# Optimization experiments

Measured on AMD Instinct MI355X. Metric: run time of the kernel, lower is better.

The kernel has to match this reference:

```python
import jax, jax.numpy as jnp
import numpy as np

S, N, DIM = 16384, 4096, 512
EPS = 1e-12

def _l2_normalize(x):
    return x / (jnp.linalg.norm(x, axis=-1, keepdims=True) + EPS)

def setup_inputs() -> dict:
    key = jax.random.key(0)
    k1, k2, k3 = jax.random.split(key, 3)
    img_emb_raw = jax.random.normal(k1, (S, DIM), dtype=jnp.float32)
    txt_emb_raw = jax.random.normal(k2, (N, DIM), dtype=jnp.float32)
    key_idx = jax.random.randint(k3, (S,), 0, N, dtype=jnp.int64 if jax.config.jax_enable_x64 else jnp.int32)
    log_t = jnp.asarray(0.0, dtype=jnp.float32)
    bias = jnp.asarray(0.0, dtype=jnp.float32)
    return {"img_emb_raw": img_emb_raw, "txt_emb_raw": txt_emb_raw, "key": key_idx, "log_t": log_t, "bias": bias}

def reference(img_emb_raw, txt_emb_raw, key, log_t, bias):
    s, dim = img_emb_raw.shape
    n = txt_emb_raw.shape[0]
    t = jnp.exp(log_t)
    zimg = _l2_normalize(img_emb_raw)
    ztxt = _l2_normalize(txt_emb_raw)
    # [s, n] dense similarity
    all_pairs_logits = jnp.matmul(zimg, ztxt.T) * t + bias
    true_positive_logits = all_pairs_logits[jnp.arange(s), key]
    potential_positive_losses = jax.nn.softplus(-true_positive_logits)  # [s]
    # grouped argmin over images sharing the same text key (first-min tiebreak)
    seg_min = jax.ops.segment_min(potential_positive_losses, key, num_segments=n)  # empty -> +inf
    is_best = potential_positive_losses == seg_min[key]
    cand_idx = jnp.where(is_best, jnp.arange(s), s)
    sel = jax.ops.segment_min(cand_idx, key, num_segments=n)
    valid = sel < s
    selected_img_global_indices = jnp.where(valid, sel, -1)
    safe_sel = jnp.where(valid, sel, 0)
    zimg_selected = jnp.where(valid[:, None], zimg[safe_sel], jnp.zeros((), dtype=zimg.dtype))
    final_logits_matrix = jnp.matmul(zimg_selected, ztxt.T) * t + bias  # [n, n]
    final_labels = 2.0 * jnp.eye(n, dtype=final_logits_matrix.dtype) - 1.0
    loss_terms = jax.nn.softplus(-(final_labels * final_logits_matrix))
    final_loss = jnp.sum(loss_terms) / n
    return (final_loss, selected_img_global_indices, zimg, ztxt, all_pairs_logits, final_logits_matrix)
```

## Files before the change

kernel.cpp:

```cpp
#include <hip/hip_runtime.h>
#include <hip/hip_bf16.h>

#define S_IMG 16384
#define N_TXT 4096
#define DIM   512
#define KDIM  512

typedef __attribute__((ext_vector_type(8))) short bf16x8;
typedef __attribute__((ext_vector_type(4))) float f32x4;

__device__ __forceinline__ short f2bf(float f) {
  unsigned u = __float_as_uint(f);
  u += 0x7FFFu + ((u >> 16) & 1u);
  return (short)(u >> 16);
}

__device__ __forceinline__ float softplus_f(float x) {
  return fmaxf(x, 0.0f) + log1pf(expf(-fabsf(x)));
}

__global__ __launch_bounds__(256) void init_kernel(
    unsigned long long* __restrict__ packed, float* __restrict__ out_loss) {
  const int i = blockIdx.x * 256 + threadIdx.x;
  packed[i] = 0xFFFFFFFFFFFFFFFFull;
  if (i == 0) out_loss[0] = 0.0f;
}

__global__ __launch_bounds__(256) void normalize_kernel(
    const float* __restrict__ in, float* __restrict__ outf,
    short* __restrict__ outb) {
  const int w = threadIdx.x >> 6, l = threadIdx.x & 63;
  const size_t row = (size_t)blockIdx.x * 4 + w;
  const float4* r4 = (const float4*)(in + row * DIM);
  float4 a = r4[l], b = r4[l + 64];
  float s = a.x*a.x + a.y*a.y + a.z*a.z + a.w*a.w
          + b.x*b.x + b.y*b.y + b.z*b.z + b.w*b.w;
#pragma unroll
  for (int off = 32; off; off >>= 1) s += __shfl_xor(s, off, 64);
  const float inv = 1.0f / (sqrtf(s) + 1e-12f);
  a.x *= inv; a.y *= inv; a.z *= inv; a.w *= inv;
  b.x *= inv; b.y *= inv; b.z *= inv; b.w *= inv;
  float4* o4 = (float4*)(outf + row * DIM);
  o4[l] = a; o4[l + 64] = b;
  int2 pa, pb;
  pa.x = (f2bf(a.x) & 0xFFFF) | ((int)f2bf(a.y) << 16);
  pa.y = (f2bf(a.z) & 0xFFFF) | ((int)f2bf(a.w) << 16);
  pb.x = (f2bf(b.x) & 0xFFFF) | ((int)f2bf(b.y) << 16);
  pb.y = (f2bf(b.z) & 0xFFFF) | ((int)f2bf(b.w) << 16);
  ((int2*)(outb + row * DIM))[l]       = pa;
  ((int2*)(outb + row * DIM + 256))[l] = pb;
}

__global__ __launch_bounds__(256) void tp_select_kernel(
    const float* __restrict__ zimg, const float* __restrict__ ztxt,
    const int* __restrict__ key, unsigned long long* __restrict__ packed,
    const float* __restrict__ logt_p, const float* __restrict__ bias_p) {
  const int w = threadIdx.x >> 6, l = threadIdx.x & 63;
  const int i = blockIdx.x * 4 + w;
  const int k = key[i];
  const float4* zi = (const float4*)(zimg + (size_t)i * DIM);
  const float4* zt = (const float4*)(ztxt + (size_t)k * DIM);
  float4 a0 = zi[l], a1 = zi[l + 64], b0 = zt[l], b1 = zt[l + 64];
  float s = a0.x*b0.x + a0.y*b0.y + a0.z*b0.z + a0.w*b0.w
          + a1.x*b1.x + a1.y*b1.y + a1.z*b1.z + a1.w*b1.w;
#pragma unroll
  for (int off = 32; off; off >>= 1) s += __shfl_xor(s, off, 64);
  if (l == 0) {
    const float t  = expf(logt_p[0]);
    const float tp = s * t + bias_p[0];
    const float loss = softplus_f(-tp);
    const unsigned long long p =
        ((unsigned long long)__float_as_uint(loss) << 32) | (unsigned)i;
    atomicMin(&packed[k], p);
  }
}

__global__ __launch_bounds__(256) void gather_kernel(
    const unsigned long long* __restrict__ packed, float* __restrict__ out_idx,
    const short* __restrict__ zimgb, short* __restrict__ zselb) {
  const int w = threadIdx.x >> 6, l = threadIdx.x & 63;
  const int n = blockIdx.x * 4 + w;
  const unsigned long long p = packed[n];
  int4 v = {0, 0, 0, 0};
  float f = -1.0f;
  if (p != 0xFFFFFFFFFFFFFFFFull) {
    const int sel = (int)(p & 0xFFFFFFFFull);
    f = (float)sel;
    v = ((const int4*)(zimgb + (size_t)sel * DIM))[l];
  }
  ((int4*)(zselb + (size_t)n * DIM))[l] = v;
  if (l == 0) out_idx[n] = f;
}

__global__ __launch_bounds__(256) void gemm_merged(
    const short* __restrict__ Aimg, const short* __restrict__ Asel,
    const short* __restrict__ B, float* __restrict__ Cap,
    float* __restrict__ Cfl, const float* __restrict__ logt_p,
    const float* __restrict__ bias_p, float* __restrict__ loss_out) {
  __shared__ alignas(16) short As[128 * 32];
  __shared__ alignas(16) short Bs[128 * 32];
  __shared__ float red[4];

  const int t = threadIdx.x;
  const int w = t >> 6, l = t & 63;
  const int wm = w >> 1, wn = w & 1;
  const int bn = blockIdx.x * 128;
  const bool fuse = (blockIdx.y >= 128);
  const int bm = (fuse ? (blockIdx.y - 128) : blockIdx.y) * 128;
  const short* A = fuse ? Asel : Aimg;
  float* C = fuse ? Cfl : Cap;
  const int fr = l & 15, quad = l >> 4;

  const int srow_base = (w << 4) + (l >> 2);
  const int sq = l & 3;

  f32x4 acc[4][4] = {};

  for (int k0 = 0; k0 < KDIM; k0 += 32) {
    __syncthreads();
#pragma unroll
    for (int c = 0; c < 2; ++c) {
      const int row = c * 64 + srow_base;
      const int qg = sq ^ ((row >> 1) & 3);
      const short* gpa = A + (size_t)(bm + row) * KDIM + k0 + qg * 8;
      const short* lpa = &As[(c * 64 + (w << 4)) * 32];
      __builtin_amdgcn_global_load_lds(
          (const __attribute__((address_space(1))) void*)gpa,
          (__attribute__((address_space(3))) void*)lpa, 16, 0, 0);
      const short* gpb = B + (size_t)(bn + row) * KDIM + k0 + qg * 8;
      const short* lpb = &Bs[(c * 64 + (w << 4)) * 32];
      __builtin_amdgcn_global_load_lds(
          (const __attribute__((address_space(1))) void*)gpb,
          (__attribute__((address_space(3))) void*)lpb, 16, 0, 0);
    }
    __syncthreads();

    bf16x8 af[4], bfr[4];
#pragma unroll
    for (int mi = 0; mi < 4; ++mi) {
      const int ar = wm * 64 + mi * 16 + fr;
      af[mi] = *(const bf16x8*)&As[ar * 32 + (quad ^ ((ar >> 1) & 3)) * 8];
      const int br = wn * 64 + mi * 16 + fr;
      bfr[mi] = *(const bf16x8*)&Bs[br * 32 + (quad ^ ((br >> 1) & 3)) * 8];
    }
#pragma unroll
    for (int mi = 0; mi < 4; ++mi)
#pragma unroll
      for (int nj = 0; nj < 4; ++nj)
        acc[mi][nj] = __builtin_amdgcn_mfma_f32_16x16x32_bf16(
            af[mi], bfr[nj], acc[mi][nj], 0, 0, 0);
  }

  const float tt = expf(logt_p[0]);
  const float bb = bias_p[0];
  float lsum = 0.0f;
#pragma unroll
  for (int mi = 0; mi < 4; ++mi) {
#pragma unroll
    for (int nj = 0; nj < 4; ++nj) {
      const int grow0 = bm + wm * 64 + mi * 16 + quad * 4;
      const int gcol  = bn + wn * 64 + nj * 16 + fr;
      f32x4 a = acc[mi][nj];
#pragma unroll
      for (int r = 0; r < 4; ++r) {
        const float v = a[r] * tt + bb;
        C[(size_t)(grow0 + r) * N_TXT + gcol] = v;
        if (fuse) {
          const float lab = (grow0 + r == gcol) ? 1.0f : -1.0f;
          lsum += softplus_f(-lab * v);
        }
      }
    }
  }
  if (fuse) {
#pragma unroll
    for (int off = 32; off; off >>= 1) lsum += __shfl_xor(lsum, off, 64);
    if (l == 0) red[w] = lsum;
    __syncthreads();
    if (t == 0)
      atomicAdd(loss_out, (red[0] + red[1] + red[2] + red[3]) * (1.0f / N_TXT));
  }
}

extern "C" void kernel_launch(void* const* d_in, const int* in_sizes, int n_in,
                              void* d_out, int out_size, void* d_ws, size_t ws_size,
                              hipStream_t stream) {
  const float* img  = (const float*)d_in[0];
  const float* txt  = (const float*)d_in[1];
  const int*   key  = (const int*)d_in[2];
  const float* logt = (const float*)d_in[3];
  const float* bias = (const float*)d_in[4];

  float* out    = (float*)d_out;
  float* o_loss = out;
  float* o_sel  = out + 1;
  float* o_zimg = o_sel + N_TXT;
  float* o_ztxt = o_zimg + (size_t)S_IMG * DIM;
  float* o_ap   = o_ztxt + (size_t)N_TXT * DIM;
  float* o_fl   = o_ap + (size_t)S_IMG * N_TXT;

  char* ws = (char*)d_ws;
  short* zimgb = (short*)ws;
  short* ztxtb = (short*)(ws + (size_t)S_IMG * DIM * 2);
  short* zselb = (short*)(ws + (size_t)(S_IMG + N_TXT) * DIM * 2);
  unsigned long long* packed =
      (unsigned long long*)(ws + (size_t)(S_IMG + 2 * N_TXT) * DIM * 2);

  init_kernel<<<N_TXT / 256, 256, 0, stream>>>(packed, o_loss);
  normalize_kernel<<<S_IMG / 4, 256, 0, stream>>>(img, o_zimg, zimgb);
  normalize_kernel<<<N_TXT / 4, 256, 0, stream>>>(txt, o_ztxt, ztxtb);
  tp_select_kernel<<<S_IMG / 4, 256, 0, stream>>>(o_zimg, o_ztxt, key, packed,
                                                  logt, bias);
  gather_kernel<<<N_TXT / 4, 256, 0, stream>>>(packed, o_sel, zimgb, zselb);
  gemm_merged<<<dim3(N_TXT / 128, S_IMG / 128 + N_TXT / 128), 256, 0, stream>>>(
      zimgb, zselb, ztxtb, o_ap, o_fl, logt, bias, o_loss);
}
```

Measured before the change: 576.7 us.

## Fuse image normalize with positive scoring and rework GEMM into pipelined 256x256 tiles

```diff
diff --git a/kernel.cpp b/kernel.cpp
--- a/kernel.cpp
+++ b/kernel.cpp
@@ -51,26 +51,45 @@
   ((int2*)(outb + row * DIM + 256))[l] = pb;
 }
 
-__global__ __launch_bounds__(256) void tp_select_kernel(
-    const float* __restrict__ zimg, const float* __restrict__ ztxt,
+__global__ __launch_bounds__(256) void normalize_img_tp_kernel(
+    const float* __restrict__ in, float* __restrict__ outf,
+    short* __restrict__ outb, const float* __restrict__ ztxt,
     const int* __restrict__ key, unsigned long long* __restrict__ packed,
     const float* __restrict__ logt_p, const float* __restrict__ bias_p) {
   const int w = threadIdx.x >> 6, l = threadIdx.x & 63;
-  const int i = blockIdx.x * 4 + w;
-  const int k = key[i];
-  const float4* zi = (const float4*)(zimg + (size_t)i * DIM);
+  const size_t row = (size_t)blockIdx.x * 4 + w;
+  const float4* r4 = (const float4*)(in + row * DIM);
+  float4 a = r4[l], b = r4[l + 64];
+  float s = a.x*a.x + a.y*a.y + a.z*a.z + a.w*a.w
+          + b.x*b.x + b.y*b.y + b.z*b.z + b.w*b.w;
+#pragma unroll
+  for (int off = 32; off; off >>= 1) s += __shfl_xor(s, off, 64);
+  const float inv = 1.0f / (sqrtf(s) + 1e-12f);
+  a.x *= inv; a.y *= inv; a.z *= inv; a.w *= inv;
+  b.x *= inv; b.y *= inv; b.z *= inv; b.w *= inv;
+  float4* o4 = (float4*)(outf + row * DIM);
+  o4[l] = a; o4[l + 64] = b;
+  int2 pa, pb;
+  pa.x = (f2bf(a.x) & 0xFFFF) | ((int)f2bf(a.y) << 16);
+  pa.y = (f2bf(a.z) & 0xFFFF) | ((int)f2bf(a.w) << 16);
+  pb.x = (f2bf(b.x) & 0xFFFF) | ((int)f2bf(b.y) << 16);
+  pb.y = (f2bf(b.z) & 0xFFFF) | ((int)f2bf(b.w) << 16);
+  ((int2*)(outb + row * DIM))[l]       = pa;
+  ((int2*)(outb + row * DIM + 256))[l] = pb;
+
+  const int k = key[row];
   const float4* zt = (const float4*)(ztxt + (size_t)k * DIM);
-  float4 a0 = zi[l], a1 = zi[l + 64], b0 = zt[l], b1 = zt[l + 64];
-  float s = a0.x*b0.x + a0.y*b0.y + a0.z*b0.z + a0.w*b0.w
-          + a1.x*b1.x + a1.y*b1.y + a1.z*b1.z + a1.w*b1.w;
-#pragma unroll
-  for (int off = 32; off; off >>= 1) s += __shfl_xor(s, off, 64);
+  float4 c0 = zt[l], c1 = zt[l + 64];
+  float d = a.x*c0.x + a.y*c0.y + a.z*c0.z + a.w*c0.w
+          + b.x*c1.x + b.y*c1.y + b.z*c1.z + b.w*c1.w;
+#pragma unroll
+  for (int off = 32; off; off >>= 1) d += __shfl_xor(d, off, 64);
   if (l == 0) {
     const float t  = expf(logt_p[0]);
-    const float tp = s * t + bias_p[0];
+    const float tp = d * t + bias_p[0];
     const float loss = softplus_f(-tp);
     const unsigned long long p =
-        ((unsigned long long)__float_as_uint(loss) << 32) | (unsigned)i;
+        ((unsigned long long)__float_as_uint(loss) << 32) | (unsigned)row;
     atomicMin(&packed[k], p);
   }
 }
@@ -92,79 +111,108 @@
   if (l == 0) out_idx[n] = f;
 }
 
-__global__ __launch_bounds__(256) void gemm_merged(
+__global__ __launch_bounds__(512, 2) void gemm_merged(
     const short* __restrict__ Aimg, const short* __restrict__ Asel,
     const short* __restrict__ B, float* __restrict__ Cap,
     float* __restrict__ Cfl, const float* __restrict__ logt_p,
     const float* __restrict__ bias_p, float* __restrict__ loss_out) {
-  __shared__ alignas(16) short As[128 * 32];
-  __shared__ alignas(16) short Bs[128 * 32];
-  __shared__ float red[4];
-
-  const int t = threadIdx.x;
-  const int w = t >> 6, l = t & 63;
-  const int wm = w >> 1, wn = w & 1;
-  const int bn = blockIdx.x * 128;
-  const bool fuse = (blockIdx.y >= 128);
-  const int bm = (fuse ? (blockIdx.y - 128) : blockIdx.y) * 128;
+  __shared__ alignas(16) short As[4][8192];
+  __shared__ alignas(16) short Bs[4][8192];
+  __shared__ float red[8];
+
+  const int t  = threadIdx.x;
+  const int w  = t >> 6, l = t & 63;
+  const int wm = w >> 2, wn = w & 3;
+  const int fr = l & 15, quad = l >> 4;
+
+  int lin = blockIdx.y * 16 + blockIdx.x;
+  lin = (lin & 7) * 160 + (lin >> 3);
+  const int bx = lin & 15, by = lin >> 4;
+
+  const bool fuse = (by >= 64);
+  const int bm = (fuse ? by - 64 : by) << 8;
+  const int bn = bx << 8;
   const short* A = fuse ? Asel : Aimg;
   float* C = fuse ? Cfl : Cap;
-  const int fr = l & 15, quad = l >> 4;
-
-  const int srow_base = (w << 4) + (l >> 2);
-  const int sq = l & 3;
-
-  f32x4 acc[4][4] = {};
-
-  for (int k0 = 0; k0 < KDIM; k0 += 32) {
-    __syncthreads();
-#pragma unroll
-    for (int c = 0; c < 2; ++c) {
-      const int row = c * 64 + srow_base;
-      const int qg = sq ^ ((row >> 1) & 3);
-      const short* gpa = A + (size_t)(bm + row) * KDIM + k0 + qg * 8;
-      const short* lpa = &As[(c * 64 + (w << 4)) * 32];
-      __builtin_amdgcn_global_load_lds(
-          (const __attribute__((address_space(1))) void*)gpa,
-          (__attribute__((address_space(3))) void*)lpa, 16, 0, 0);
-      const short* gpb = B + (size_t)(bn + row) * KDIM + k0 + qg * 8;
-      const short* lpb = &Bs[(c * 64 + (w << 4)) * 32];
-      __builtin_amdgcn_global_load_lds(
-          (const __attribute__((address_space(1))) void*)gpb,
-          (__attribute__((address_space(3))) void*)lpb, 16, 0, 0);
-    }
-    __syncthreads();
-
-    bf16x8 af[4], bfr[4];
-#pragma unroll
-    for (int mi = 0; mi < 4; ++mi) {
-      const int ar = wm * 64 + mi * 16 + fr;
-      af[mi] = *(const bf16x8*)&As[ar * 32 + (quad ^ ((ar >> 1) & 3)) * 8];
-      const int br = wn * 64 + mi * 16 + fr;
-      bfr[mi] = *(const bf16x8*)&Bs[br * 32 + (quad ^ ((br >> 1) & 3)) * 8];
-    }
-#pragma unroll
-    for (int mi = 0; mi < 4; ++mi)
-#pragma unroll
-      for (int nj = 0; nj < 4; ++nj)
-        acc[mi][nj] = __builtin_amdgcn_mfma_f32_16x16x32_bf16(
-            af[mi], bfr[nj], acc[mi][nj], 0, 0, 0);
-  }
+
+  const int srow   = t >> 2;
+  const int schunk = ((t & 3) ^ (srow & 3)) << 3;
+  const short* Ag = A + (size_t)(bm + srow) * KDIM + schunk;
+  const short* Bg = B + (size_t)(bn + srow) * KDIM + schunk;
+  const int sdst = w << 9;
+
+  const int rchunk = (quad ^ (fr & 3)) << 3;
+  const int abase = (wm * 128 + fr) * 32 + rchunk;
+  const int bbase = (wn * 64 + fr) * 32 + rchunk;
+
+  f32x4 acc[8][4] = {};
+
+  auto stage = [&](int tile) {
+    const int p = tile & 3;
+    const int k0 = tile << 5;
+    const short* ga = Ag + k0;
+    const short* gb = Bg + k0;
+    short* la = &As[p][sdst];
+    short* lb = &Bs[p][sdst];
+    __builtin_amdgcn_global_load_lds(
+        (const __attribute__((address_space(1))) void*)ga,
+        (__attribute__((address_space(3))) void*)la, 16, 0, 0);
+    __builtin_amdgcn_global_load_lds(
+        (const __attribute__((address_space(1))) void*)(ga + (size_t)128 * KDIM),
+        (__attribute__((address_space(3))) void*)(la + 4096), 16, 0, 0);
+    __builtin_amdgcn_global_load_lds(
+        (const __attribute__((address_space(1))) void*)gb,
+        (__attribute__((address_space(3))) void*)lb, 16, 0, 0);
+    __builtin_amdgcn_global_load_lds(
+        (const __attribute__((address_space(1))) void*)(gb + (size_t)128 * KDIM),
+        (__attribute__((address_space(3))) void*)(lb + 4096), 16, 0, 0);
+  };
+
+  stage(0); stage(1); stage(2);
+
+#define TILE(T, WN)                                                           \
+  {                                                                           \
+    asm volatile("s_waitcnt vmcnt(" #WN ")" ::: "memory");                    \
+    __builtin_amdgcn_s_barrier();                                             \
+    if ((T) + 3 < 16) stage((T) + 3);                                         \
+    const short* Ab = &As[(T) & 3][abase];                                    \
+    const short* Bb = &Bs[(T) & 3][bbase];                                    \
+    bf16x8 af[8], bq[4];                                                      \
+    _Pragma("unroll")                                                         \
+    for (int mi = 0; mi < 8; ++mi) af[mi] = *(const bf16x8*)(Ab + mi * 512);  \
+    _Pragma("unroll")                                                         \
+    for (int nj = 0; nj < 4; ++nj) bq[nj] = *(const bf16x8*)(Bb + nj * 512);  \
+    __builtin_amdgcn_s_setprio(1);                                            \
+    _Pragma("unroll")                                                         \
+    for (int mi = 0; mi < 8; ++mi)                                            \
+      _Pragma("unroll")                                                       \
+      for (int nj = 0; nj < 4; ++nj)                                          \
+        acc[mi][nj] = __builtin_amdgcn_mfma_f32_16x16x32_bf16(                \
+            af[mi], bq[nj], acc[mi][nj], 0, 0, 0);                            \
+    __builtin_amdgcn_s_setprio(0);                                            \
+    asm volatile("s_waitcnt lgkmcnt(0)" ::: "memory");                        \
+  }
+
+#pragma unroll
+  for (int T = 0; T < 14; ++T) TILE(T, 8)
+  TILE(14, 4)
+  TILE(15, 0)
+#undef TILE
 
   const float tt = expf(logt_p[0]);
   const float bb = bias_p[0];
   float lsum = 0.0f;
 #pragma unroll
-  for (int mi = 0; mi < 4; ++mi) {
+  for (int mi = 0; mi < 8; ++mi) {
 #pragma unroll
     for (int nj = 0; nj < 4; ++nj) {
-      const int grow0 = bm + wm * 64 + mi * 16 + quad * 4;
+      const int grow0 = bm + wm * 128 + mi * 16 + quad * 4;
       const int gcol  = bn + wn * 64 + nj * 16 + fr;
       f32x4 a = acc[mi][nj];
 #pragma unroll
       for (int r = 0; r < 4; ++r) {
         const float v = a[r] * tt + bb;
-        C[(size_t)(grow0 + r) * N_TXT + gcol] = v;
+        __builtin_nontemporal_store(v, &C[(size_t)(grow0 + r) * N_TXT + gcol]);
         if (fuse) {
           const float lab = (grow0 + r == gcol) ? 1.0f : -1.0f;
           lsum += softplus_f(-lab * v);
@@ -177,8 +225,12 @@
     for (int off = 32; off; off >>= 1) lsum += __shfl_xor(lsum, off, 64);
     if (l == 0) red[w] = lsum;
     __syncthreads();
-    if (t == 0)
-      atomicAdd(loss_out, (red[0] + red[1] + red[2] + red[3]) * (1.0f / N_TXT));
+    if (t == 0) {
+      float s2 = 0.0f;
+#pragma unroll
+      for (int i = 0; i < 8; ++i) s2 += red[i];
+      atomicAdd(loss_out, s2 * (1.0f / N_TXT));
+    }
   }
 }
 
@@ -207,11 +259,10 @@
       (unsigned long long*)(ws + (size_t)(S_IMG + 2 * N_TXT) * DIM * 2);
 
   init_kernel<<<N_TXT / 256, 256, 0, stream>>>(packed, o_loss);
-  normalize_kernel<<<S_IMG / 4, 256, 0, stream>>>(img, o_zimg, zimgb);
   normalize_kernel<<<N_TXT / 4, 256, 0, stream>>>(txt, o_ztxt, ztxtb);
-  tp_select_kernel<<<S_IMG / 4, 256, 0, stream>>>(o_zimg, o_ztxt, key, packed,
-                                                  logt, bias);
+  normalize_img_tp_kernel<<<S_IMG / 4, 256, 0, stream>>>(
+      img, o_zimg, zimgb, o_ztxt, key, packed, logt, bias);
   gather_kernel<<<N_TXT / 4, 256, 0, stream>>>(packed, o_sel, zimgb, zselb);
-  gemm_merged<<<dim3(N_TXT / 128, S_IMG / 128 + N_TXT / 128), 256, 0, stream>>>(
+  gemm_merged<<<dim3(N_TXT / 256, S_IMG / 256 + N_TXT / 256), 512, 0, stream>>>(
       zimgb, zselb, ztxtb, o_ap, o_fl, logt, bias, o_loss);
 }
```

After: 766.1 us. +32.8%, slower.
